# Kernel tuning notes

Hardware: AMD Instinct MI355X
Metric: run time of the kernel (lower is better)

The kernel has to match this reference:

```python
import jax, jax.numpy as jnp
import numpy as np

B, IN, OUT = 16384, 4096, 4096


def setup_inputs() -> dict:
    key = jax.random.key(0)
    k1, k2, k3 = jax.random.split(key, 3)
    x = jax.random.normal(k1, (B, IN), dtype=jnp.float32)
    full_precision = jax.random.normal(k2, (OUT, IN), dtype=jnp.float32) * 0.02
    bias = jax.random.normal(k3, (OUT,), dtype=jnp.float32) * 0.02
    return {"x": x, "full_precision": full_precision, "bias": bias}


def reference(x, full_precision, bias):
    # In-place param preprocessing from the torch module:
    # center each weight row, then clamp to [-1, 1].
    fp = full_precision - jnp.mean(full_precision, axis=1, keepdims=True)
    fp = jnp.clip(fp, -1.0, 1.0)
    # BinActive: sign of the activations (dropout_ratio == 0, so no dropout).
    xb = jnp.sign(x)
    # Binary weight: sign(fp) scaled by per-output-row mean absolute value.
    mean_val = jnp.mean(jnp.abs(fp), axis=1, keepdims=True)  # [OUT, 1]
    w = jnp.sign(fp) * mean_val                               # [OUT, IN]
    # Dense linear: [B, IN] @ [IN, OUT] + [OUT]
    return xb @ w.T + bias
```

## Files before the change

kernel.cpp:

```cpp
#include <hip/hip_runtime.h>
#include <cstdint>

#define B_SZ   16384
#define IN_SZ  4096
#define OUT_SZ 4096

typedef int int4v  __attribute__((ext_vector_type(4)));
typedef int int16v __attribute__((ext_vector_type(16)));

__device__ __forceinline__ int sgn8(float v) { return (v > 0.f) - (v < 0.f); }

__global__ __launch_bounds__(256) void wprep_kernel(const float* __restrict__ fp,
                                                    int8_t* __restrict__ wb,
                                                    float* __restrict__ alpha) {
    __shared__ float red[4];
    const int o = blockIdx.x;
    const int t = threadIdx.x;
    const float4* row = (const float4*)(fp + (size_t)o * IN_SZ);

    float4 v[4];
    float s = 0.f;
#pragma unroll
    for (int i = 0; i < 4; ++i) {
        v[i] = row[t + i * 256];
        s += (v[i].x + v[i].y) + (v[i].z + v[i].w);
    }
#pragma unroll
    for (int off = 32; off > 0; off >>= 1) s += __shfl_down(s, off, 64);
    if ((t & 63) == 0) red[t >> 6] = s;
    __syncthreads();
    const float mean = (red[0] + red[1] + red[2] + red[3]) * (1.f / IN_SZ);
    __syncthreads();

    int* wrow = (int*)(wb + (size_t)o * IN_SZ);
    float a = 0.f;
#pragma unroll
    for (int i = 0; i < 4; ++i) {
        const float dx = v[i].x - mean, dy = v[i].y - mean;
        const float dz = v[i].z - mean, dw = v[i].w - mean;
        a += fminf(fabsf(dx), 1.f) + fminf(fabsf(dy), 1.f)
           + fminf(fabsf(dz), 1.f) + fminf(fabsf(dw), 1.f);
        const int p = (sgn8(dx) & 0xff) | ((sgn8(dy) & 0xff) << 8)
                    | ((sgn8(dz) & 0xff) << 16) | (sgn8(dw) << 24);
        wrow[t + i * 256] = p;
    }
#pragma unroll
    for (int off = 32; off > 0; off >>= 1) a += __shfl_down(a, off, 64);
    if ((t & 63) == 0) red[t >> 6] = a;
    __syncthreads();
    if (t == 0) alpha[o] = (red[0] + red[1] + red[2] + red[3]) * (1.f / IN_SZ);
}

__global__ __launch_bounds__(256) void xprep_kernel(const float* __restrict__ x,
                                                    int8_t* __restrict__ xb) {
    const size_t i = ((size_t)blockIdx.x * 256 + threadIdx.x) * 2;
    const float4 v0 = ((const float4*)x)[i];
    const float4 v1 = ((const float4*)x)[i + 1];
    int2 p;
    p.x = (sgn8(v0.x) & 0xff) | ((sgn8(v0.y) & 0xff) << 8)
        | ((sgn8(v0.z) & 0xff) << 16) | (sgn8(v0.w) << 24);
    p.y = (sgn8(v1.x) & 0xff) | ((sgn8(v1.y) & 0xff) << 8)
        | ((sgn8(v1.z) & 0xff) << 16) | (sgn8(v1.w) << 24);
    ((int2*)xb)[i / 2] = p;
}

__global__ __launch_bounds__(256, 3) void gemm_kernel(const int8_t* __restrict__ Xb,
                                                      const int8_t* __restrict__ Wb,
                                                      const float* __restrict__ alpha,
                                                      const float* __restrict__ bias,
                                                      float* __restrict__ out) {
    __shared__ __align__(16) int8_t As[2][256 * 64];
    __shared__ __align__(16) int8_t Bs[2][128 * 64];

    const int tid  = threadIdx.x;
    const int lane = tid & 63;
    const int wave = tid >> 6;

    const int bid     = blockIdx.x;
    const int logical = (bid & 7) * 256 + (bid >> 3);
    const int group   = logical >> 7;
    const int rem     = logical & 127;
    const int tm = group * 4 + (rem & 3);
    const int tn = rem >> 2;

    const int wm = (wave >> 1) * 128;
    const int wn = (wave & 1) * 64;

    const int srow = lane >> 2;
    const int scol = ((lane & 3) ^ ((lane >> 3) & 3)) << 4;
    const int8_t* gA = Xb + (size_t)(tm * 256 + wave * 64 + srow) * IN_SZ + scol;
    const int8_t* gB = Wb + (size_t)(tn * 128 + wave * 32 + srow) * IN_SZ + scol;

    int16v acc[4][2] = {};

    const int frow  = lane & 31;
    const int khalf = lane >> 5;
    const int fxor  = (lane >> 1) & 3;

    auto stage = [&](int bb, int k0) {
#pragma unroll
        for (int j = 0; j < 4; ++j)
            __builtin_amdgcn_global_load_lds(
                (const __attribute__((address_space(1))) uint32_t*)(gA + k0 + (size_t)j * 16 * IN_SZ),
                (__attribute__((address_space(3))) uint32_t*)(&As[bb][(wave * 64 + j * 16) * 64]),
                16, 0, 0);
#pragma unroll
        for (int j = 0; j < 2; ++j)
            __builtin_amdgcn_global_load_lds(
                (const __attribute__((address_space(1))) uint32_t*)(gB + k0 + (size_t)j * 16 * IN_SZ),
                (__attribute__((address_space(3))) uint32_t*)(&Bs[bb][(wave * 32 + j * 16) * 64]),
                16, 0, 0);
    };

    stage(0, 0);
    __syncthreads();

    int bb = 0;
    for (int k0 = 0; k0 < IN_SZ; k0 += 64) {
        if (k0 + 64 < IN_SZ) stage(bb ^ 1, k0 + 64);

#pragma unroll
        for (int s = 0; s < 2; ++s) {
            const int chunk = ((s * 2 + khalf) ^ fxor) << 4;
            int4v a[4], b[2];
#pragma unroll
            for (int i = 0; i < 4; ++i)
                a[i] = *(const int4v*)(&As[bb][(wm + i * 32 + frow) * 64 + chunk]);
#pragma unroll
            for (int j = 0; j < 2; ++j)
                b[j] = *(const int4v*)(&Bs[bb][(wn + j * 32 + frow) * 64 + chunk]);
#pragma unroll
            for (int i = 0; i < 4; ++i)
#pragma unroll
                for (int j = 0; j < 2; ++j)
                    acc[i][j] = __builtin_amdgcn_mfma_i32_32x32x32_i8(a[i], b[j], acc[i][j], 0, 0, 0);
        }
        __syncthreads();
        bb ^= 1;
    }

    const int col = lane & 31;
    const int rbase = 4 * (lane >> 5);
#pragma unroll
    for (int j = 0; j < 2; ++j) {
        const int o = tn * 128 + wn + j * 32 + col;
        const float al = alpha[o];
        const float bi = bias[o];
#pragma unroll
        for (int i = 0; i < 4; ++i) {
            const size_t mbase = (size_t)(tm * 256 + wm + i * 32);
#pragma unroll
            for (int r = 0; r < 16; ++r) {
                const int row = (r & 3) + 8 * (r >> 2) + rbase;
                __builtin_nontemporal_store(al * (float)acc[i][j][r] + bi,
                                            &out[(mbase + row) * OUT_SZ + o]);
            }
        }
    }
}

extern "C" void kernel_launch(void* const* d_in, const int* in_sizes, int n_in,
                              void* d_out, int out_size, void* d_ws, size_t ws_size,
                              hipStream_t stream) {
    const float* x    = (const float*)d_in[0];
    const float* fp   = (const float*)d_in[1];
    const float* bias = (const float*)d_in[2];
    float* out = (float*)d_out;

    int8_t* xb    = (int8_t*)d_ws;
    int8_t* wb    = xb + (size_t)B_SZ * IN_SZ;
    float*  alpha = (float*)(wb + (size_t)OUT_SZ * IN_SZ);

    hipLaunchKernelGGL(wprep_kernel, dim3(OUT_SZ), dim3(256), 0, stream, fp, wb, alpha);
    hipLaunchKernelGGL(xprep_kernel, dim3(B_SZ * IN_SZ / 2048), dim3(256), 0, stream, x, xb);
    hipLaunchKernelGGL(gemm_kernel, dim3((B_SZ / 256) * (OUT_SZ / 128)), dim3(256), 0, stream,
                       xb, wb, alpha, bias, out);
}
```

Measured before the change: 756.1 us.

## Triple-buffer GEMM LDS staging with explicit vmcnt waits and MFMA priority

Moves the int8 GEMM from double-buffered to triple-buffered LDS staging, prefetching two tiles ahead and using explicit s_waitcnt vmcnt counts plus raw barriers in place of __syncthreads. It also raises wave priority around the MFMA block with s_setprio. The aim is to hide global-to-LDS load latency better. The cost is 72KB of LDS per block, so launch bounds drop from 3 to 2 blocks per CU, lowering occupancy, and the hand-counted waitcnts are fragile if the compiler emits other memory ops.

```diff
diff --git a/kernel.cpp b/kernel.cpp
--- a/kernel.cpp
+++ b/kernel.cpp
@@ -64,13 +64,13 @@
     ((int2*)xb)[i / 2] = p;
 }
 
-__global__ __launch_bounds__(256, 3) void gemm_kernel(const int8_t* __restrict__ Xb,
+__global__ __launch_bounds__(256, 2) void gemm_kernel(const int8_t* __restrict__ Xb,
                                                       const int8_t* __restrict__ Wb,
                                                       const float* __restrict__ alpha,
                                                       const float* __restrict__ bias,
                                                       float* __restrict__ out) {
-    __shared__ __align__(16) int8_t As[2][256 * 64];
-    __shared__ __align__(16) int8_t Bs[2][128 * 64];
+    __shared__ __align__(16) int8_t As[3][256 * 64];
+    __shared__ __align__(16) int8_t Bs[3][128 * 64];
 
     const int tid  = threadIdx.x;
     const int lane = tid & 63;
@@ -97,46 +97,64 @@
     const int khalf = lane >> 5;
     const int fxor  = (lane >> 1) & 3;
 
-    auto stage = [&](int bb, int k0) {
+    auto stage = [&](int c, int k0) {
 #pragma unroll
         for (int j = 0; j < 4; ++j)
             __builtin_amdgcn_global_load_lds(
                 (const __attribute__((address_space(1))) uint32_t*)(gA + k0 + (size_t)j * 16 * IN_SZ),
-                (__attribute__((address_space(3))) uint32_t*)(&As[bb][(wave * 64 + j * 16) * 64]),
+                (__attribute__((address_space(3))) uint32_t*)(&As[c][(wave * 64 + j * 16) * 64]),
                 16, 0, 0);
 #pragma unroll
         for (int j = 0; j < 2; ++j)
             __builtin_amdgcn_global_load_lds(
                 (const __attribute__((address_space(1))) uint32_t*)(gB + k0 + (size_t)j * 16 * IN_SZ),
-                (__attribute__((address_space(3))) uint32_t*)(&Bs[bb][(wave * 32 + j * 16) * 64]),
+                (__attribute__((address_space(3))) uint32_t*)(&Bs[c][(wave * 32 + j * 16) * 64]),
                 16, 0, 0);
     };
 
+    const int NT = IN_SZ / 64;
     stage(0, 0);
-    __syncthreads();
+    stage(1, 64);
+    stage(2, 128);
+    asm volatile("s_waitcnt vmcnt(12)" ::: "memory");
+    __builtin_amdgcn_s_barrier();
 
-    int bb = 0;
-    for (int k0 = 0; k0 < IN_SZ; k0 += 64) {
-        if (k0 + 64 < IN_SZ) stage(bb ^ 1, k0 + 64);
-
+    int cur = 0;
+    for (int t = 0; t < NT; ++t) {
+        const int8_t* Ab = As[cur];
+        const int8_t* Bb = Bs[cur];
 #pragma unroll
         for (int s = 0; s < 2; ++s) {
             const int chunk = ((s * 2 + khalf) ^ fxor) << 4;
             int4v a[4], b[2];
 #pragma unroll
             for (int i = 0; i < 4; ++i)
-                a[i] = *(const int4v*)(&As[bb][(wm + i * 32 + frow) * 64 + chunk]);
+                a[i] = *(const int4v*)(Ab + (wm + i * 32 + frow) * 64 + chunk);
 #pragma unroll
             for (int j = 0; j < 2; ++j)
-                b[j] = *(const int4v*)(&Bs[bb][(wn + j * 32 + frow) * 64 + chunk]);
+                b[j] = *(const int4v*)(Bb + (wn + j * 32 + frow) * 64 + chunk);
+            __builtin_amdgcn_s_setprio(1);
 #pragma unroll
             for (int i = 0; i < 4; ++i)
 #pragma unroll
                 for (int j = 0; j < 2; ++j)
                     acc[i][j] = __builtin_amdgcn_mfma_i32_32x32x32_i8(a[i], b[j], acc[i][j], 0, 0, 0);
+            __builtin_amdgcn_s_setprio(0);
         }
-        __syncthreads();
-        bb ^= 1;
+        asm volatile("s_waitcnt lgkmcnt(0)" ::: "memory");
+        __builtin_amdgcn_s_barrier();
+        if (t + 3 < NT) {
+            stage(cur, (t + 3) * 64);
+            asm volatile("s_waitcnt vmcnt(12)" ::: "memory");
+        } else if (t + 2 < NT) {
+            asm volatile("s_waitcnt vmcnt(6)" ::: "memory");
+        } else if (t + 1 < NT) {
+            asm volatile("s_waitcnt vmcnt(0)" ::: "memory");
+        }
+        __builtin_amdgcn_s_barrier();
+        __builtin_amdgcn_sched_barrier(0);
+        cur = cur + 1;
+        if (cur == 3) cur = 0;
     }
 
     const int col = lane & 31;
```

Result: no change. 767.8 us (+1.6%).
